# Kernel optimization log

Measured on AMD Instinct MI355X. Metric: run time of the kernel, lower is better.

## Reference

```python
import jax, jax.numpy as jnp
import numpy as np

EPS = 1e-7
PROJ_EPS = 1e-5
MAX_TANH_ARG = 15.0
COMBINE_RELS_WEIGHT = 0.1


def _norm(x):
    return jnp.sqrt(jnp.sum(x * x, axis=-1, keepdims=True))


def log_map_zero(x):
    n = _norm(x)
    nc = jnp.clip(n, EPS, 1.0 - PROJ_EPS)
    return jnp.arctanh(nc) * x / jnp.maximum(n, EPS)


def exp_map_zero(v):
    n = jnp.maximum(_norm(v), EPS)
    return jnp.tanh(jnp.minimum(n, MAX_TANH_ARG)) * v / n


def hyperbolic_projection(x):
    n = jnp.maximum(_norm(x), EPS)
    maxnorm = 1.0 - PROJ_EPS
    return x * jnp.minimum(1.0, maxnorm / n)


def mobius_addition(u, v):
    uv = jnp.sum(u * v, axis=-1, keepdims=True)
    u2 = jnp.sum(u * u, axis=-1, keepdims=True)
    v2 = jnp.sum(v * v, axis=-1, keepdims=True)
    num = (1.0 + 2.0 * uv + v2) * u + (1.0 - u2) * v
    den = 1.0 + 2.0 * uv + u2 * v2
    return num / jnp.maximum(den, EPS)


def setup_inputs() -> dict:
    key = jax.random.key(0)
    ks = jax.random.split(key, 9)
    N, R, D, E = 50000, 1000, 128, 640000
    # embeddings start well inside the Poincare ball
    ents = 0.01 * jax.random.normal(ks[0], (N, D), dtype=jnp.float32)
    rels = 0.01 * jax.random.normal(ks[1], (R, D), dtype=jnp.float32)
    W_ent = jax.random.normal(ks[2], (D, D), dtype=jnp.float32) * (1.0 / np.sqrt(D))
    bias_vec = jnp.zeros((1, D), dtype=jnp.float32)
    ent_row = jax.random.randint(ks[3], (E,), 0, N, dtype=jnp.int32)
    ent_col = jax.random.randint(ks[4], (E,), 0, N, dtype=jnp.int32)
    rel_row = jax.random.randint(ks[5], (E,), 0, N, dtype=jnp.int32)
    rel_val = jax.random.randint(ks[6], (E,), 0, R, dtype=jnp.int32)
    near_rels_num = (1.0 + jax.random.randint(ks[7], (N,), 0, 32, dtype=jnp.int32)).astype(jnp.float32)
    return {"ents_embed_input": ents, "rels_embed_input": rels, "W_ent": W_ent,
            "bias_vec": bias_vec, "ent_row": ent_row, "ent_col": ent_col,
            "rel_row": rel_row, "rel_val": rel_val, "near_rels_num": near_rels_num}


def reference(ents_embed_input, rels_embed_input, W_ent, bias_vec,
              ent_row, ent_col, rel_row, rel_val, near_rels_num):
    N = ents_embed_input.shape[0]
    # tangent-space map + linear transform
    ents_tan = log_map_zero(ents_embed_input)          # [N, D]
    h = ents_tan @ W_ent                                # [N, D]
    # GAT-style sparse attention on adjacency (scores are detached in original)
    hd = jax.lax.stop_gradient(h)
    scores = jnp.sum(hd[ent_row] * hd[ent_col], axis=-1)  # [E]
    m = jax.ops.segment_max(scores, ent_row, num_segments=N)
    e = jnp.exp(scores - m[ent_row])
    denom = jax.ops.segment_sum(e, ent_row, num_segments=N)
    alpha = e / jnp.maximum(denom[ent_row], EPS)           # [E]
    near_ents = jax.ops.segment_sum(alpha[:, None] * h[ent_col], ent_row, num_segments=N)
    # relation neighborhood mean (gather + scatter-sum)
    edge_emb = rels_embed_input[rel_val]                   # [E, D]
    near_rels = jax.ops.segment_sum(edge_emb, rel_row, num_segments=N)
    near_rels = near_rels / near_rels_num[:, None]
    out = hyperbolic_projection(exp_map_zero(near_ents + COMBINE_RELS_WEIGHT * near_rels))
    b = hyperbolic_projection(exp_map_zero(bias_vec))
    out = hyperbolic_projection(mobius_addition(out, b))
    return out
```

## Files before the change

kernel.cpp:

```cpp
#include <hip/hip_runtime.h>
#include <hip/hip_fp16.h>
#include <math.h>

#define EPS 1e-7f
#define PROJ_EPS 1e-5f
#define MAXNORM (1.0f - PROJ_EPS)
#define D_DIM 128
#define CAP 48
#define PSHIFT 7
#define NPART 392
#define PCAP 2048
#define CHUNK 4096
#define NCONV 32
#define ATS 136
#define WTS 136
#define PRE0_SMEM (64 * 132 * 4)
#define MAIN_SMEM (64 * ATS * 2 + 128 * WTS * 2 + 256)

typedef _Float16 f16;
typedef __attribute__((ext_vector_type(4))) _Float16 f16x4;
typedef __attribute__((ext_vector_type(8))) _Float16 f16x8;
typedef __attribute__((ext_vector_type(4))) float f32x4;

__device__ inline float wred(float v) {
    #pragma unroll
    for (int o = 32; o; o >>= 1) v += __shfl_xor(v, o, 64);
    return v;
}
__device__ inline float gred(float v) {
    v += __shfl_xor(v, 1, 64);
    v += __shfl_xor(v, 2, 64);
    v += __shfl_xor(v, 4, 64);
    v += __shfl_xor(v, 8, 64);
    return v;
}
__device__ inline void gred4(float& a, float& b, float& c, float& d) {
    a += __shfl_xor(a, 1, 64);  b += __shfl_xor(b, 1, 64);
    c += __shfl_xor(c, 1, 64);  d += __shfl_xor(d, 1, 64);
    a += __shfl_xor(a, 2, 64);  b += __shfl_xor(b, 2, 64);
    c += __shfl_xor(c, 2, 64);  d += __shfl_xor(d, 2, 64);
    a += __shfl_xor(a, 4, 64);  b += __shfl_xor(b, 4, 64);
    c += __shfl_xor(c, 4, 64);  d += __shfl_xor(d, 4, 64);
    a += __shfl_xor(a, 8, 64);  b += __shfl_xor(b, 8, 64);
    c += __shfl_xor(c, 8, 64);  d += __shfl_xor(d, 8, 64);
}
__device__ inline __half2 bc_h2(unsigned int u) { return *(__half2*)&u; }
__device__ inline unsigned int bc_u32(__half2 h) { return *(unsigned int*)&h; }

typedef _Float16 h2v __attribute__((ext_vector_type(2)));
__device__ inline h2v as_h2v(unsigned int u) { union { unsigned int u; h2v h; } c; c.u = u; return c.h; }

__device__ inline float dot8d(uint4 a, uint4 v) {
#if __has_builtin(__builtin_amdgcn_fdot2)
    float s = __builtin_amdgcn_fdot2(as_h2v(a.x), as_h2v(v.x), 0.f, false);
    s = __builtin_amdgcn_fdot2(as_h2v(a.y), as_h2v(v.y), s, false);
    s = __builtin_amdgcn_fdot2(as_h2v(a.z), as_h2v(v.z), s, false);
    s = __builtin_amdgcn_fdot2(as_h2v(a.w), as_h2v(v.w), s, false);
    return s;
#else
    __half2 t = __hmul2(bc_h2(a.x), bc_h2(v.x));
    t = __hfma2(bc_h2(a.y), bc_h2(v.y), t);
    t = __hfma2(bc_h2(a.z), bc_h2(v.z), t);
    t = __hfma2(bc_h2(a.w), bc_h2(v.w), t);
    return __low2float(t) + __high2float(t);
#endif
}
__device__ inline void acc8h(__half2* A, float w, uint4 v) {
    __half2 w2 = __float2half2_rn(w);
    A[0] = __hfma2(w2, bc_h2(v.x), A[0]);
    A[1] = __hfma2(w2, bc_h2(v.y), A[1]);
    A[2] = __hfma2(w2, bc_h2(v.z), A[2]);
    A[3] = __hfma2(w2, bc_h2(v.w), A[3]);
}
__device__ inline void add8h(__half2* A, uint4 v) {
    A[0] = __hadd2(A[0], bc_h2(v.x));
    A[1] = __hadd2(A[1], bc_h2(v.y));
    A[2] = __hadd2(A[2], bc_h2(v.z));
    A[3] = __hadd2(A[3], bc_h2(v.w));
}

__global__ __launch_bounds__(256) void k_pre0(
    const float* __restrict__ W, f16* __restrict__ Wt_h,
    const float* __restrict__ bias, float* __restrict__ bws,
    int* __restrict__ cursors) {
    __shared__ alignas(16) unsigned char smem[PRE0_SMEM];
    int tid = threadIdx.x;

    if (blockIdx.x == 0) {
        for (int i = tid; i < 2 * NPART; i += 256) cursors[i] = 0;
        if (tid < 64) {
            int l = tid;
            float2 bv = ((const float2*)bias)[l];
            float bn = fmaxf(sqrtf(wred(bv.x * bv.x + bv.y * bv.y)), EPS);
            float gb = tanhf(fminf(bn, 15.f)) / bn;
            float bx = gb * bv.x, by = gb * bv.y;
            float nb = fmaxf(sqrtf(wred(bx * bx + by * by)), EPS);
            float pb = fminf(1.f, MAXNORM / nb);
            bx *= pb; by *= pb;
            ((float2*)bws)[l] = make_float2(bx, by);
            float v2 = wred(bx * bx + by * by);
            if (l == 0) bws[128] = v2;
        }
        return;
    }

    float* lts = (float*)smem;
    unsigned int* wt_u = (unsigned int*)Wt_h;
    for (int pass = 0; pass < 2; pass++) {
        #pragma unroll
        for (int i = 0; i < 8; i++) {
            int flat = (tid + i * 256) * 4;
            int kr = flat >> 7, cc = flat & 127;
            float4 x = *(const float4*)(W + (size_t)(pass * 64 + kr) * D_DIM + cc);
            *(float4*)&lts[kr * 132 + cc] = x;
        }
        __syncthreads();
        #pragma unroll
        for (int i = 0; i < 16; i++) {
            int flat2 = tid + i * 256;
            int c = flat2 >> 5, kp = flat2 & 31;
            float lo = lts[(2 * kp) * 132 + c];
            float hi = lts[(2 * kp + 1) * 132 + c];
            wt_u[c * 64 + pass * 32 + kp] = bc_u32(__float22half2_rn(make_float2(lo, hi)));
        }
        __syncthreads();
    }
}

__global__ __launch_bounds__(256) void k_main(
    const float* __restrict__ ents, const f16* __restrict__ Wt_h,
    __half* __restrict__ hh,
    const int* __restrict__ er, const int* __restrict__ ec,
    const int* __restrict__ rr, const int* __restrict__ rv,
    int* __restrict__ part_e, int* __restrict__ part_r,
    int* __restrict__ cursors,
    const float* __restrict__ rels, f16* __restrict__ rels_h, int relsN4,
    int N, int E, int nGemm, int nChunk) {
    __shared__ alignas(16) unsigned char smem[MAIN_SMEM];
    int tid = threadIdx.x;
    int bid = blockIdx.x;

    if (bid < nGemm) {
        f16* atile = (f16*)smem;
        f16* wtile = (f16*)(smem + 64 * ATS * 2);
        float* fac = (float*)(smem + 64 * ATS * 2 + 128 * WTS * 2);
        int lane = tid & 63;
        int wv = tid >> 6;
        int r0 = bid * 64;

        #pragma unroll
        for (int i = 0; i < 8; i++) {
            int flat = (tid + i * 256) * 4;
            int rr2 = flat >> 7, cc = flat & 127;
            float4 x = make_float4(0.f, 0.f, 0.f, 0.f);
            if (r0 + rr2 < N) x = *(const float4*)(ents + (size_t)(r0 + rr2) * D_DIM + cc);
            f16x4 v4 = {(f16)x.x, (f16)x.y, (f16)x.z, (f16)x.w};
            *(f16x4*)&atile[rr2 * ATS + cc] = v4;
            float s = x.x * x.x + x.y * x.y + x.z * x.z + x.w * x.w;
            s += __shfl_xor(s, 1, 64);
            s += __shfl_xor(s, 2, 64);
            s += __shfl_xor(s, 4, 64);
            s += __shfl_xor(s, 8, 64);
            s += __shfl_xor(s, 16, 64);
            if ((lane & 31) == 0) fac[rr2] = s;
        }
        #pragma unroll
        for (int i = 0; i < 8; i++) {
            int flat4 = tid + i * 256;
            int c = flat4 >> 4, off = (flat4 & 15) * 8;
            uint4 u = ((const uint4*)Wt_h)[flat4];
            *(uint4*)&wtile[c * WTS + off] = u;
        }
        __syncthreads();

        if (tid < 64) {
            float n = sqrtf(fac[tid]);
            float ncl = fminf(fmaxf(n, EPS), MAXNORM);
            float at = 0.5f * logf((1.f + ncl) / (1.f - ncl));
            fac[tid] = at / fmaxf(n, EPS);
        }
        __syncthreads();

        int l15 = lane & 15, kseg = lane >> 4;
        int arow = wv * 16 + l15;

        f32x4 acc[8];
        #pragma unroll
        for (int ct = 0; ct < 8; ct++) acc[ct] = (f32x4){0.f, 0.f, 0.f, 0.f};

        #pragma unroll
        for (int ks = 0; ks < 4; ks++) {
            int k0 = ks * 32 + kseg * 8;
            f16x8 af = *(const f16x8*)&atile[arow * ATS + k0];
            #pragma unroll
            for (int ct = 0; ct < 8; ct++) {
                f16x8 bf = *(const f16x8*)&wtile[(ct * 16 + l15) * WTS + k0];
                acc[ct] = __builtin_amdgcn_mfma_f32_16x16x32_f16(af, bf, acc[ct], 0, 0, 0);
            }
        }
        __syncthreads();

        #pragma unroll
        for (int rg = 0; rg < 4; rg++) {
            int m = wv * 16 + kseg * 4 + rg;
            float fc = fac[m];
            #pragma unroll
            for (int ct = 0; ct < 8; ct++) {
                atile[m * ATS + ct * 16 + l15] = (f16)(acc[ct][rg] * fc);
            }
        }
        __syncthreads();

        #pragma unroll
        for (int i = 0; i < 4; i++) {
            int flat4 = tid + i * 256;
            int rr2 = flat4 >> 4, off = (flat4 & 15) * 8;
            if (r0 + rr2 < N) {
                uint4 u = *(const uint4*)&atile[rr2 * ATS + off];
                *(uint4*)((char*)hh + ((size_t)(r0 + rr2)) * 256 + off * 2) = u;
            }
        }
        return;
    }

    if (bid < nGemm + NCONV) {
        int gtid = (bid - nGemm) * 256 + tid;
        for (int i = gtid; i < relsN4; i += NCONV * 256) {
            float4 x = ((const float4*)rels)[i];
            uint2 u;
            u.x = bc_u32(__float22half2_rn(make_float2(x.x, x.y)));
            u.y = bc_u32(__float22half2_rn(make_float2(x.z, x.w)));
            ((uint2*)rels_h)[i] = u;
        }
        return;
    }

    int pid = bid - nGemm - NCONV;
    int pair = (pid >= nChunk) ? 1 : 0;
    int chunk = pair ? pid - nChunk : pid;
    int* hist = (int*)smem;
    int* dlt  = hist + NPART;
    int* sc   = dlt + NPART;
    int* st   = sc + 256;
    const int* rsrc = pair ? rr : er;
    const int* psrc = pair ? rv : ec;
    int* part = pair ? part_r : part_e;
    int* cur  = cursors + pair * NPART;
    int e0 = chunk * CHUNK;
    int n = min(CHUNK, E - e0);

    for (int i = tid; i < NPART; i += 256) hist[i] = 0;
    __syncthreads();

    int myr[16], rk[16];
    #pragma unroll
    for (int i = 0; i < 16; i++) {
        int e = e0 + tid + i * 256;
        if (e < E) {
            int r = rsrc[e];
            myr[i] = r;
            rk[i] = atomicAdd(&hist[r >> PSHIFT], 1);
        } else myr[i] = -1;
    }
    __syncthreads();

    int h0 = (2 * tid < NPART) ? hist[2 * tid] : 0;
    int h1 = (2 * tid + 1 < NPART) ? hist[2 * tid + 1] : 0;
    int s = h0 + h1;
    sc[tid] = s;
    __syncthreads();
    for (int off = 1; off < 256; off <<= 1) {
        int v = (tid >= off) ? sc[tid - off] : 0;
        __syncthreads();
        sc[tid] += v;
        __syncthreads();
    }
    int excl = sc[tid] - s;
    if (2 * tid < NPART) dlt[2 * tid] = excl;
    if (2 * tid + 1 < NPART) dlt[2 * tid + 1] = excl + h0;
    __syncthreads();

    #pragma unroll
    for (int i = 0; i < 16; i++) {
        if (myr[i] >= 0) {
            int e = e0 + tid + i * 256;
            unsigned int pk = ((unsigned int)myr[i] << 16) | (unsigned int)(psrc[e] & 0xFFFF);
            st[dlt[myr[i] >> PSHIFT] + rk[i]] = (int)pk;
        }
    }
    __syncthreads();

    for (int p = tid; p < NPART; p += 256) {
        int len = hist[p];
        if (len > 0) {
            int g = atomicAdd(&cur[p], len);
            if (g + len > PCAP) g = PCAP - len;
            if (g < 0) g = 0;
            dlt[p] = p * PCAP + g - dlt[p];
        }
    }
    __syncthreads();

    for (int i = tid; i < n; i += 256) {
        unsigned int v = (unsigned int)st[i];
        int p = (int)(v >> 16) >> PSHIFT;
        part[dlt[p] + i] = (int)v;
    }
}

__global__ __launch_bounds__(256) void k_bucket(
    const int* __restrict__ part_e, const int* __restrict__ part_r,
    const int* __restrict__ cursors,
    unsigned short* __restrict__ pay_e, unsigned short* __restrict__ pay_r,
    int* __restrict__ cnt, int N) {
    __shared__ int bcnt[128];
    __shared__ unsigned short bb[128 * CAP];
    int tid = threadIdx.x;
    int p = blockIdx.x;
    int pair = blockIdx.y;
    const int* part = (pair ? part_r : part_e) + (size_t)p * PCAP;
    unsigned short* pay = pair ? pay_r : pay_e;
    int* cnt_out = cnt + (size_t)pair * N;
    int n = min(cursors[pair * NPART + p], PCAP);

    if (tid < 128) bcnt[tid] = 0;
    __syncthreads();

    for (int i = tid; i < n; i += 256) {
        unsigned int v = (unsigned int)part[i];
        int rl = (int)((v >> 16) & 127);
        int slot = atomicAdd(&bcnt[rl], 1);
        if (slot < CAP) bb[rl * CAP + slot] = (unsigned short)(v & 0xFFFF);
    }
    __syncthreads();

    int rbase = p * 128;
    uint4* gdst = (uint4*)(pay + (size_t)rbase * CAP);
    const uint4* gsrc = (const uint4*)bb;
    for (int i = tid; i < 768; i += 256) gdst[i] = gsrc[i];
    if (tid < 128 && rbase + tid < N) cnt_out[rbase + tid] = bcnt[tid];
}

__global__ __launch_bounds__(256) void k_row(
    const __half* __restrict__ hh, const __half* __restrict__ rels_h,
    const float* __restrict__ bws, const float* __restrict__ nrn,
    const int* __restrict__ cnt, const unsigned short* __restrict__ pay_e,
    const unsigned short* __restrict__ pay_r,
    float* __restrict__ out, int N) {
    int wv = threadIdx.x >> 6, lane = threadIdx.x & 63;
    int sub = lane >> 4, sl = lane & 15;
    int gb = lane & 48;
    int r = blockIdx.x * 16 + wv * 4 + sub;
    bool valid = r < N;
    int rc = valid ? r : 0;

    const char* hB = (const char*)hh + sl * 16;
    const char* rB = (const char*)rels_h + sl * 16;
    uint4 hraw = *(const uint4*)(hB + ((size_t)rc << 8));
    float nrn_v = nrn[rc];

    int deg  = valid ? min(cnt[rc], CAP) : 0;
    int degr = valid ? min(cnt[N + rc], CAP) : 0;

    size_t be = (size_t)rc * CAP;
    int i0e = (sl      < deg) ? (int)pay_e[be + sl]      : 0;
    int i1e = (sl + 16 < deg) ? (int)pay_e[be + sl + 16] : 0;
    int i2e = (sl + 32 < deg) ? (int)pay_e[be + sl + 32] : 0;
    int i0r = (sl      < degr) ? (int)pay_r[be + sl]      : 0;
    int i1r = (sl + 16 < degr) ? (int)pay_r[be + sl + 16] : 0;
    int i2r = (sl + 32 < degr) ? (int)pay_r[be + sl + 32] : 0;

    int md = deg;
    md = max(md, __shfl_xor(md, 16, 64));
    md = max(md, __shfl_xor(md, 32, 64));
    int mdr = degr;
    mdr = max(mdr, __shfl_xor(mdr, 16, 64));
    mdr = max(mdr, __shfl_xor(mdr, 32, 64));

    __half2 aA[4] = {bc_h2(0u), bc_h2(0u), bc_h2(0u), bc_h2(0u)};
    float den = 0.f;

    auto att4 = [&](int idxreg, int base) {
        #pragma unroll
        for (int k = 0; k < 16; k += 4) {
            int t = base + k;
            if (t >= md) break;
            int c0 = __shfl(idxreg, gb | k);
            int c1 = __shfl(idxreg, gb | (k + 1));
            int c2 = __shfl(idxreg, gb | (k + 2));
            int c3 = __shfl(idxreg, gb | (k + 3));
            uint4 v0 = *(const uint4*)(hB + ((size_t)c0 << 8));
            uint4 v1 = *(const uint4*)(hB + ((size_t)c1 << 8));
            uint4 v2 = *(const uint4*)(hB + ((size_t)c2 << 8));
            uint4 v3 = *(const uint4*)(hB + ((size_t)c3 << 8));
            float s0 = dot8d(hraw, v0);
            float s1 = dot8d(hraw, v1);
            float s2 = dot8d(hraw, v2);
            float s3 = dot8d(hraw, v3);
            gred4(s0, s1, s2, s3);
            float w0 = (t     < deg) ? __expf(s0) : 0.f;
            float w1 = (t + 1 < deg) ? __expf(s1) : 0.f;
            float w2 = (t + 2 < deg) ? __expf(s2) : 0.f;
            float w3 = (t + 3 < deg) ? __expf(s3) : 0.f;
            den += (w0 + w1) + (w2 + w3);
            acc8h(aA, w0, v0);
            acc8h(aA, w1, v1);
            acc8h(aA, w2, v2);
            acc8h(aA, w3, v3);
        }
    };
    att4(i0e, 0);
    if (md > 16) att4(i1e, 16);
    if (md > 32) att4(i2e, 32);

    __half2 rA[4] = {bc_h2(0u), bc_h2(0u), bc_h2(0u), bc_h2(0u)};
    auto rel4 = [&](int idxreg, int base) {
        #pragma unroll
        for (int k = 0; k < 16; k += 4) {
            int t = base + k;
            if (t >= mdr) break;
            int c0 = __shfl(idxreg, gb | k);
            int c1 = __shfl(idxreg, gb | (k + 1));
            int c2 = __shfl(idxreg, gb | (k + 2));
            int c3 = __shfl(idxreg, gb | (k + 3));
            uint4 v0 = *(const uint4*)(rB + ((size_t)c0 << 8));
            uint4 v1 = *(const uint4*)(rB + ((size_t)c1 << 8));
            uint4 v2 = *(const uint4*)(rB + ((size_t)c2 << 8));
            uint4 v3 = *(const uint4*)(rB + ((size_t)c3 << 8));
            if (t     < degr) add8h(rA, v0);
            if (t + 1 < degr) add8h(rA, v1);
            if (t + 2 < degr) add8h(rA, v2);
            if (t + 3 < degr) add8h(rA, v3);
        }
    };
    rel4(i0r, 0);
    if (mdr > 16) rel4(i1r, 16);
    if (mdr > 32) rel4(i2r, 32);

    float inv  = 1.f / fmaxf(den, EPS);
    float innr = 0.1f / nrn_v;
    float2 a0 = __half22float2(aA[0]), a1 = __half22float2(aA[1]);
    float2 a2 = __half22float2(aA[2]), a3 = __half22float2(aA[3]);
    float2 r0f = __half22float2(rA[0]), r1f = __half22float2(rA[1]);
    float2 r2f = __half22float2(rA[2]), r3f = __half22float2(rA[3]);
    float v0 = a0.x * inv + r0f.x * innr, v1 = a0.y * inv + r0f.y * innr;
    float v2_ = a1.x * inv + r1f.x * innr, v3 = a1.y * inv + r1f.y * innr;
    float v4 = a2.x * inv + r2f.x * innr, v5 = a2.y * inv + r2f.y * innr;
    float v6 = a3.x * inv + r3f.x * innr, v7 = a3.y * inv + r3f.y * innr;

    float pn = v0*v0 + v1*v1 + v2_*v2_ + v3*v3 + v4*v4 + v5*v5 + v6*v6 + v7*v7;
    pn = gred(pn);
    float sq = sqrtf(pn);
    float nn = fmaxf(sq, EPS);
    float tt = __expf(2.f * fminf(nn, 15.f));
    float g = (tt - 1.f) / ((tt + 1.f) * nn);
    float n2 = fmaxf(g * sq, EPS);
    float pf = fminf(1.f, MAXNORM / n2);
    float gp = g * pf;
    float o0 = gp*v0, o1 = gp*v1, o2 = gp*v2_, o3 = gp*v3;
    float o4 = gp*v4, o5 = gp*v5, o6 = gp*v6, o7 = gp*v7;
    float un = n2 * pf;
    float u2 = un * un;

    const float4* bp = (const float4*)(bws + sl * 8);
    float4 b0 = bp[0], b1 = bp[1];
    float bv2 = bws[128];
    float puv = o0*b0.x + o1*b0.y + o2*b0.z + o3*b0.w
              + o4*b1.x + o5*b1.y + o6*b1.z + o7*b1.w;
    puv = gred(puv);
    float ca = 1.f + 2.f * puv + bv2;
    float cb = 1.f - u2;
    float idm = 1.f / fmaxf(1.f + 2.f * puv + u2 * bv2, EPS);
    float x0 = (ca*o0 + cb*b0.x) * idm, x1 = (ca*o1 + cb*b0.y) * idm;
    float x2 = (ca*o2 + cb*b0.z) * idm, x3 = (ca*o3 + cb*b0.w) * idm;
    float x4 = (ca*o4 + cb*b1.x) * idm, x5 = (ca*o5 + cb*b1.y) * idm;
    float x6 = (ca*o6 + cb*b1.z) * idm, x7 = (ca*o7 + cb*b1.w) * idm;
    float pr = x0*x0 + x1*x1 + x2*x2 + x3*x3 + x4*x4 + x5*x5 + x6*x6 + x7*x7;
    pr = gred(pr);
    float n3 = fmaxf(sqrtf(pr), EPS);
    float pf3 = fminf(1.f, MAXNORM / n3);

    if (valid) {
        float4* op = (float4*)(out + (size_t)r * D_DIM + sl * 8);
        op[0] = make_float4(x0 * pf3, x1 * pf3, x2 * pf3, x3 * pf3);
        op[1] = make_float4(x4 * pf3, x5 * pf3, x6 * pf3, x7 * pf3);
    }
}

extern "C" void kernel_launch(void* const* d_in, const int* in_sizes, int n_in,
                              void* d_out, int out_size, void* d_ws, size_t ws_size,
                              hipStream_t stream) {
    const float* ents = (const float*)d_in[0];
    const float* rels = (const float*)d_in[1];
    const float* W    = (const float*)d_in[2];
    const float* bias = (const float*)d_in[3];
    const int* er = (const int*)d_in[4];
    const int* ec = (const int*)d_in[5];
    const int* rr = (const int*)d_in[6];
    const int* rv = (const int*)d_in[7];
    const float* nrn = (const float*)d_in[8];
    int N = in_sizes[0] / D_DIM;
    int R = in_sizes[1] / D_DIM;
    int E = in_sizes[4];
    float* out = (float*)d_out;

    char* p = (char*)d_ws;
    auto alloc = [&](size_t bytes) {
        char* q = p;
        p += (bytes + 255) & ~(size_t)255;
        return q;
    };
    const int PADN = NPART * 128;
    __half* hh     = (__half*)alloc((size_t)N * D_DIM * 2);
    f16* rels_h    = (f16*)alloc((size_t)R * D_DIM * 2);
    f16* Wt_h      = (f16*)alloc((size_t)D_DIM * D_DIM * 2);
    int* cnt    = (int*)alloc((size_t)2 * N * 4);
    unsigned short* pay_e = (unsigned short*)alloc((size_t)PADN * CAP * 2);
    unsigned short* pay_r = (unsigned short*)alloc((size_t)PADN * CAP * 2);
    int* part_e = (int*)alloc((size_t)NPART * PCAP * 4);
    int* part_r = (int*)alloc((size_t)NPART * PCAP * 4);
    int* cursors = (int*)alloc((size_t)2 * NPART * 4);
    float* bws   = (float*)alloc((size_t)132 * 4);

    int nGemm = (N + 63) / 64;
    int nChunk = (E + CHUNK - 1) / CHUNK;
    int relsN4 = R * D_DIM / 4;

    k_pre0<<<2, 256, 0, stream>>>(W, Wt_h, bias, bws, cursors);

    k_main<<<nGemm + NCONV + 2 * nChunk, 256, 0, stream>>>(
        ents, Wt_h, hh, er, ec, rr, rv, part_e, part_r, cursors,
        rels, rels_h, relsN4, N, E, nGemm, nChunk);

    k_bucket<<<dim3(NPART, 2), 256, 0, stream>>>(part_e, part_r, cursors, pay_e, pay_r, cnt, N);

    k_row<<<(N + 15) / 16, 256, 0, stream>>>(
        hh, (const __half*)rels_h, bws, nrn, cnt, pay_e, pay_r, out, N);
}
```

Measured before the change: 74.60 us.

## Sort rows by entity-edge degree within partitions to balance row-kernel wavefronts

In the bucketing kernel, each 128-row partition ranks its rows by entity-neighbour count and writes a permutation. The row kernel then processes rows in that order, so the four rows sharing a wavefront have similar degrees and the max-degree loop bounds waste fewer lanes. The cost is an extra indirection load per row, scattered writes to the output, and a small O(128) ranking loop per partition. Relation degrees are not considered in the ordering.

```diff
diff --git a/kernel.cpp b/kernel.cpp
--- a/kernel.cpp
+++ b/kernel.cpp
@@ -312,8 +312,9 @@
     const int* __restrict__ part_e, const int* __restrict__ part_r,
     const int* __restrict__ cursors,
     unsigned short* __restrict__ pay_e, unsigned short* __restrict__ pay_r,
-    int* __restrict__ cnt, int N) {
+    int* __restrict__ cnt, int* __restrict__ perm, int N) {
     __shared__ int bcnt[128];
+    __shared__ int keys[128];
     __shared__ unsigned short bb[128 * CAP];
     int tid = threadIdx.x;
     int p = blockIdx.x;
@@ -339,30 +340,44 @@
     const uint4* gsrc = (const uint4*)bb;
     for (int i = tid; i < 768; i += 256) gdst[i] = gsrc[i];
     if (tid < 128 && rbase + tid < N) cnt_out[rbase + tid] = bcnt[tid];
+
+    if (pair == 0) {
+        int nrows = min(128, N - rbase);
+        if (nrows > 0) {
+            if (tid < 128) keys[tid] = bcnt[tid] * 128 + tid;
+            __syncthreads();
+            if (tid < nrows) {
+                int mykey = keys[tid];
+                int rank = 0;
+                for (int j = 0; j < nrows; j++) rank += (keys[j] < mykey) ? 1 : 0;
+                perm[rbase + rank] = rbase + tid;
+            }
+        }
+    }
 }
 
 __global__ __launch_bounds__(256) void k_row(
     const __half* __restrict__ hh, const __half* __restrict__ rels_h,
     const float* __restrict__ bws, const float* __restrict__ nrn,
     const int* __restrict__ cnt, const unsigned short* __restrict__ pay_e,
-    const unsigned short* __restrict__ pay_r,
+    const unsigned short* __restrict__ pay_r, const int* __restrict__ perm,
     float* __restrict__ out, int N) {
     int wv = threadIdx.x >> 6, lane = threadIdx.x & 63;
     int sub = lane >> 4, sl = lane & 15;
     int gb = lane & 48;
-    int r = blockIdx.x * 16 + wv * 4 + sub;
-    bool valid = r < N;
-    int rc = valid ? r : 0;
+    int g = blockIdx.x * 16 + wv * 4 + sub;
+    bool valid = g < N;
+    int r = valid ? perm[g] : 0;
 
     const char* hB = (const char*)hh + sl * 16;
     const char* rB = (const char*)rels_h + sl * 16;
-    uint4 hraw = *(const uint4*)(hB + ((size_t)rc << 8));
-    float nrn_v = nrn[rc];
-
-    int deg  = valid ? min(cnt[rc], CAP) : 0;
-    int degr = valid ? min(cnt[N + rc], CAP) : 0;
-
-    size_t be = (size_t)rc * CAP;
+    uint4 hraw = *(const uint4*)(hB + ((size_t)r << 8));
+    float nrn_v = nrn[r];
+
+    int deg  = valid ? min(cnt[r], CAP) : 0;
+    int degr = valid ? min(cnt[N + r], CAP) : 0;
+
+    size_t be = (size_t)r * CAP;
     int i0e = (sl      < deg) ? (int)pay_e[be + sl]      : 0;
     int i1e = (sl + 16 < deg) ? (int)pay_e[be + sl + 16] : 0;
     int i2e = (sl + 32 < deg) ? (int)pay_e[be + sl + 32] : 0;
@@ -453,10 +468,10 @@
     float sq = sqrtf(pn);
     float nn = fmaxf(sq, EPS);
     float tt = __expf(2.f * fminf(nn, 15.f));
-    float g = (tt - 1.f) / ((tt + 1.f) * nn);
-    float n2 = fmaxf(g * sq, EPS);
+    float g2 = (tt - 1.f) / ((tt + 1.f) * nn);
+    float n2 = fmaxf(g2 * sq, EPS);
     float pf = fminf(1.f, MAXNORM / n2);
-    float gp = g * pf;
+    float gp = g2 * pf;
     float o0 = gp*v0, o1 = gp*v1, o2 = gp*v2_, o3 = gp*v3;
     float o4 = gp*v4, o5 = gp*v5, o6 = gp*v6, o7 = gp*v7;
     float un = n2 * pf;
@@ -520,6 +535,7 @@
     int* part_e = (int*)alloc((size_t)NPART * PCAP * 4);
     int* part_r = (int*)alloc((size_t)NPART * PCAP * 4);
     int* cursors = (int*)alloc((size_t)2 * NPART * 4);
+    int* perm    = (int*)alloc((size_t)N * 4);
     float* bws   = (float*)alloc((size_t)132 * 4);
 
     int nGemm = (N + 63) / 64;
@@ -532,8 +548,9 @@
         ents, Wt_h, hh, er, ec, rr, rv, part_e, part_r, cursors,
         rels, rels_h, relsN4, N, E, nGemm, nChunk);
 
-    k_bucket<<<dim3(NPART, 2), 256, 0, stream>>>(part_e, part_r, cursors, pay_e, pay_r, cnt, N);
+    k_bucket<<<dim3(NPART, 2), 256, 0, stream>>>(part_e, part_r, cursors,
+                                                 pay_e, pay_r, cnt, perm, N);
 
     k_row<<<(N + 15) / 16, 256, 0, stream>>>(
-        hh, (const __half*)rels_h, bws, nrn, cnt, pay_e, pay_r, out, N);
-}
+        hh, (const __half*)rels_h, bws, nrn, cnt, pay_e, pay_r, perm, out, N);
+}
```

Result: slower. 79.40 us (+6.4%).
